# Performance work log

Measured on AMD Instinct MI355X. Metric: run time of the kernel, lower is better.

## Reference

```python
import jax, jax.numpy as jnp
import numpy as np

B, D, H, E, L = 8192, 1024, 1024, 16, 2  # batch, input_dim, exp_hidden_dim, exp_num, exp_layers


def setup_inputs() -> dict:
    key = jax.random.key(0)
    ks = jax.random.split(key, 12)
    s_in = 1.0 / np.sqrt(D)
    s_h = 1.0 / np.sqrt(H)
    return {
        "x":   jax.random.normal(ks[0], (B, D), dtype=jnp.float32),
        # per-expert embedding layer (E experts fused on leading axis)
        "W1":  jax.random.uniform(ks[1], (E, D, H), jnp.float32, -s_in, s_in),
        "b1":  jax.random.uniform(ks[2], (E, H), jnp.float32, -s_in, s_in),
        # per-expert hidden layer (shared across the L repeated blocks, as in the torch code)
        "W2":  jax.random.uniform(ks[3], (E, H, H), jnp.float32, -s_h, s_h),
        "b2":  jax.random.uniform(ks[4], (E, H), jnp.float32, -s_h, s_h),
        # per-expert output layer H -> 1
        "Wo":  jax.random.uniform(ks[5], (E, H), jnp.float32, -s_h, s_h),
        "bo":  jax.random.uniform(ks[6], (E,), jnp.float32, -s_h, s_h),
        # two gates: D -> E, softmax
        "Wg1": jax.random.uniform(ks[7], (D, E), jnp.float32, -s_in, s_in),
        "bg1": jax.random.uniform(ks[8], (E,), jnp.float32, -s_in, s_in),
        "Wg2": jax.random.uniform(ks[9], (D, E), jnp.float32, -s_in, s_in),
        "bg2": jax.random.uniform(ks[10], (E,), jnp.float32, -s_in, s_in),
    }


def reference(x, W1, b1, W2, b2, Wo, bo, Wg1, bg1, Wg2, bg2):
    # Batched experts: h [B, E, H]
    h = jax.nn.sigmoid(jnp.einsum("bd,edh->beh", x, W1) + b1)
    for _ in range(L):  # weight-shared hidden blocks (ReLU then the SAME linear)
        h = jnp.einsum("beh,ehk->bek", jax.nn.relu(h), W2) + b2
    f = jnp.einsum("beh,eh->be", h, Wo) + bo  # expert scalar outputs [B, E]
    g1 = jax.nn.softmax(x @ Wg1 + bg1, axis=-1)  # [B, E]
    g2 = jax.nn.softmax(x @ Wg2 + bg2, axis=-1)
    out1 = jnp.einsum("be,be->b", g1, f)
    out2 = jnp.einsum("be,be->b", g2, f)
    return (out1, out2)
```

## Files before the change

### kernel.cpp

```cpp
#include <hip/hip_runtime.h>
#include <hip/hip_bf16.h>
#include <cstdint>
#include <cstddef>


using half8   = __attribute__((ext_vector_type(8))) _Float16;
using floatx4 = __attribute__((ext_vector_type(4))) float;

template<int ACT>
__global__ __launch_bounds__(256, 3)
void gemm_kernel(const _Float16* __restrict__ A, const _Float16* __restrict__ Bt,
                 const float* __restrict__ bias, _Float16* __restrict__ C,
                 size_t a_estride,
                 const float* __restrict__ Wo, float* __restrict__ f, int e0)
{
    __shared__ __align__(16) _Float16 sbuf[2][16 * 512];

    const int tid  = threadIdx.x;
    const int lane = tid & 63;
    const int w    = tid >> 6;
    const int wm   = w & 1;
    const int wn   = w >> 1;

    const int g    = gridDim.z;
    const int flat = blockIdx.x + (blockIdx.y << 3) + (blockIdx.z << 9);
    const int xcd  = flat & 7;
    int s = flat >> 3;
    int le, mb_base;
    if (g <= 8) {
        const int p = 8 / g;
        le = xcd / p;
        mb_base = (xcd % p) * (64 / p);
    } else {
        le = (xcd << 1) | (s >> 9);
        s &= 511;
        mb_base = 0;
    }
    const int nb = (s >> 2) & 7;
    const int mb = mb_base + (s >> 5) * 4 + (s & 3);
    const int m0 = mb * 128;
    const int n0 = nb * 128;

    const _Float16* Ae = A   + (size_t)le * a_estride;
    const _Float16* Be = Bt  + (size_t)le * (1024ull * 1024ull);
    const float*    be = bias + (size_t)le * 1024ull;
    _Float16*       Ce = C   + (size_t)le * (8192ull * 1024ull);

    const int mtb_blk = m0 >> 4;
    const int ntb_blk = n0 >> 4;
    const int mtb = mtb_blk + wm * 4;

    const _Float16* gs[4];
#pragma unroll
    for (int u = 0; u < 4; ++u) {
        const int fidx = w * 4 + u;
        gs[u] = (fidx < 8)
            ? (Ae + (size_t)(mtb_blk + fidx) * (32 * 512) + lane * 8)
            : (Be + (size_t)(ntb_blk + (fidx - 8)) * (32 * 512) + lane * 8);
    }

    floatx4 acc[4][4];
#pragma unroll
    for (int i = 0; i < 4; ++i)
#pragma unroll
        for (int j = 0; j < 4; ++j) { floatx4 z = {0.f, 0.f, 0.f, 0.f}; acc[i][j] = z; }

    auto STAGE = [&](_Float16* buf) {
#pragma unroll
        for (int u = 0; u < 4; ++u) {
            __builtin_amdgcn_global_load_lds(
                (const __attribute__((address_space(1))) void*)gs[u],
                (__attribute__((address_space(3))) void*)(buf + (w * 4 + u) * 512),
                16, 0, 0);
            gs[u] += 512;
        }
    };
    auto COMPUTE = [&](const _Float16* buf) {
        half8 a[4], b[4];
#pragma unroll
        for (int i = 0; i < 4; ++i)
            a[i] = *(const half8*)(buf + (wm * 4 + i) * 512 + lane * 8);
#pragma unroll
        for (int j = 0; j < 4; ++j)
            b[j] = *(const half8*)(buf + 4096 + (wn * 4 + j) * 512 + lane * 8);
#pragma unroll
        for (int i = 0; i < 4; ++i)
#pragma unroll
            for (int j = 0; j < 4; ++j)
                acc[i][j] = __builtin_amdgcn_mfma_f32_16x16x32_f16(a[i], b[j], acc[i][j], 0, 0, 0);
    };

    STAGE(sbuf[0]);
    __syncthreads();
#pragma unroll 1
    for (int c = 0; c < 30; c += 2) {
        STAGE(sbuf[1]);
        COMPUTE(sbuf[0]);
        __syncthreads();
        STAGE(sbuf[0]);
        COMPUTE(sbuf[1]);
        __syncthreads();
    }
    STAGE(sbuf[1]);
    COMPUTE(sbuf[0]);
    __syncthreads();
    COMPUTE(sbuf[1]);

    const int q   = lane >> 4;
    const int l15 = lane & 15;
    float bj[4];
#pragma unroll
    for (int j = 0; j < 4; ++j) bj[j] = be[n0 + wn * 64 + j * 16 + l15];

    if (ACT == 2) {
        const float* we = Wo + (size_t)(e0 + le) * 1024;
        float wj[4];
#pragma unroll
        for (int j = 0; j < 4; ++j) wj[j] = we[n0 + wn * 64 + j * 16 + l15];
#pragma unroll
        for (int i = 0; i < 4; ++i) {
            const int mbase = m0 + wm * 64 + i * 16 + q * 4;
#pragma unroll
            for (int r = 0; r < 4; ++r) {
                float sacc = 0.f;
#pragma unroll
                for (int j = 0; j < 4; ++j)
                    sacc += fmaxf(acc[i][j][r] + bj[j], 0.0f) * wj[j];
#pragma unroll
                for (int m = 1; m < 16; m <<= 1) sacc += __shfl_xor(sacc, m, 64);
                if (l15 == 0) atomicAdd(&f[(size_t)(mbase + r) * 16 + (e0 + le)], sacc);
            }
        }
    } else {
        __syncthreads();
        _Float16* T = &sbuf[0][0] + w * (32 * 72);
        const int kcg0 = ((n0 + wn * 64) >> 5);
#pragma unroll
        for (int p = 0; p < 2; ++p) {
#pragma unroll
            for (int i2 = 0; i2 < 2; ++i2) {
                const int i = p * 2 + i2;
#pragma unroll
                for (int r = 0; r < 4; ++r) {
                    const int row = i2 * 16 + q * 4 + r;
#pragma unroll
                    for (int j = 0; j < 4; ++j) {
                        float v = acc[i][j][r] + bj[j];
                        v = 1.0f / (1.0f + __expf(-v));
                        T[row * 72 + j * 16 + l15] = (_Float16)v;
                    }
                }
            }
#pragma unroll
            for (int i2 = 0; i2 < 2; ++i2) {
                const int i = p * 2 + i2;
                const int mt = mtb + i;
#pragma unroll
                for (int kci = 0; kci < 2; ++kci) {
                    half8 v = *(const half8*)(T + (i2 * 16 + l15) * 72 + kci * 32 + q * 8);
                    *(half8*)(Ce + ((size_t)mt * 32 + kcg0 + kci) * 512 + lane * 8) = v;
                }
            }
        }
    }
}

__global__ __launch_bounds__(256)
void castx_kernel(const float* __restrict__ x, _Float16* __restrict__ xb)
{
    __shared__ _Float16 tile[64 * 72];
    const int k0 = blockIdx.x * 64;
    const int m0 = blockIdx.y * 64;
    const int tid = threadIdx.x;
    const int col4 = (tid & 15) * 4;
    const int rb   = tid >> 4;
#pragma unroll
    for (int p = 0; p < 4; ++p) {
        const int row = rb + p * 16;
        float4 a = *(const float4*)(x + (size_t)(m0 + row) * 1024 + k0 + col4);
        _Float16* d = tile + row * 72 + col4;
        d[0] = (_Float16)a.x; d[1] = (_Float16)a.y; d[2] = (_Float16)a.z; d[3] = (_Float16)a.w;
    }
    __syncthreads();
    const int lane = tid & 63, w = tid >> 6;
    const int l15 = lane & 15, q = lane >> 4;
#pragma unroll
    for (int ff = 0; ff < 2; ++ff) {
        const int fidx = w * 2 + ff;
        const int mi = fidx >> 1, kci = fidx & 1;
        half8 v = *(const half8*)(tile + (mi * 16 + l15) * 72 + kci * 32 + q * 8);
        const size_t mt = (m0 >> 4) + mi, kc = (k0 >> 5) + kci;
        *(half8*)(xb + (mt * 32 + kc) * 512 + lane * 8) = v;
    }
}

__global__ __launch_bounds__(256)
void wtr_kernel(const float* __restrict__ W1, const float* __restrict__ W2,
                _Float16* __restrict__ W1F, _Float16* __restrict__ W2F,
                const float* __restrict__ Wo, float* __restrict__ v)
{
    __shared__ _Float16 tile[64 * 73];
    const int z = blockIdx.z;
    const float* src = (z < 16) ? (W1 + (size_t)z * 1048576ull) : (W2 + (size_t)(z - 16) * 1048576ull);
    _Float16*    dst = (z < 16) ? (W1F + (size_t)z * 1048576ull) : (W2F + (size_t)(z - 16) * 1048576ull);
    const int n0 = blockIdx.x * 64;
    const int k0 = blockIdx.y * 64;
    const int tid = threadIdx.x;
    const int lane = tid & 63, w = tid >> 6;
    const int l15 = lane & 15, q = lane >> 4;

    const int col4 = l15 * 4;
    const int rbase = w * 4 + q;
    float4 a4[4];
#pragma unroll
    for (int p = 0; p < 4; ++p) {
        const int row = rbase + p * 16;
        a4[p] = *(const float4*)(src + (size_t)(k0 + row) * 1024 + n0 + col4);
        _Float16* d = tile + row * 73 + col4;
        d[0] = (_Float16)a4[p].x; d[1] = (_Float16)a4[p].y;
        d[2] = (_Float16)a4[p].z; d[3] = (_Float16)a4[p].w;
    }

    if (z >= 16) {
        const int e = z - 16;
        const float* wo = Wo + ((size_t)e << 10) + n0;
        float* ve = v + ((size_t)e << 10) + k0;
#pragma unroll
        for (int p = 0; p < 4; ++p) {
            float s = a4[p].x * wo[col4] + a4[p].y * wo[col4 + 1]
                    + a4[p].z * wo[col4 + 2] + a4[p].w * wo[col4 + 3];
            s += __shfl_xor(s, 1, 64);
            s += __shfl_xor(s, 2, 64);
            s += __shfl_xor(s, 4, 64);
            s += __shfl_xor(s, 8, 64);
            if (l15 == 0) atomicAdd(&ve[rbase + p * 16], s);
        }
    }

    __syncthreads();
#pragma unroll
    for (int ff = 0; ff < 2; ++ff) {
        const int fidx = w * 2 + ff;
        const int nti = fidx >> 1, kci = fidx & 1;
        half8 hv;
#pragma unroll
        for (int jj = 0; jj < 8; ++jj)
            hv[jj] = tile[(kci * 32 + q * 8 + jj) * 73 + nti * 16 + l15];
        const size_t nt = (n0 >> 4) + nti, kc = (k0 >> 5) + kci;
        *(half8*)(dst + (nt * 32 + kc) * 512 + lane * 8) = hv;
    }
}

__global__ __launch_bounds__(256)
void zerof_kernel(float* __restrict__ f)
{
    const size_t i = ((size_t)blockIdx.x * 256 + threadIdx.x) * 4;
    float4 z = {0.f, 0.f, 0.f, 0.f};
    *(float4*)(f + i) = z;
}

__global__ __launch_bounds__(64)
void prep_bo2_kernel(const float* __restrict__ b2, const float* __restrict__ Wo,
                     const float* __restrict__ bo, float* __restrict__ bo2)
{
    const int e = blockIdx.x;
    const int lane = threadIdx.x;
    const float* br = b2 + ((size_t)e << 10);
    const float* wo = Wo + ((size_t)e << 10);
    float s = 0.f;
#pragma unroll
    for (int t = 0; t < 16; ++t) s += br[t * 64 + lane] * wo[t * 64 + lane];
#pragma unroll
    for (int m = 1; m < 64; m <<= 1) s += __shfl_xor(s, m, 64);
    if (lane == 0) bo2[e] = s + bo[e];
}

__global__ __launch_bounds__(256)
void final_kernel(const float* __restrict__ x,
                  const float* __restrict__ Wg1, const float* __restrict__ bg1,
                  const float* __restrict__ Wg2, const float* __restrict__ bg2,
                  const float* __restrict__ f, const float* __restrict__ bo2,
                  float* __restrict__ out)
{
    const int lane = threadIdx.x & 63;
    const int w    = threadIdx.x >> 6;
    const int b    = blockIdx.x * 8 + w * 2;
    const float* xA = x + (size_t)b * 1024;
    const float* xB = xA + 1024;
    float g1A[16], g2A[16], g1B[16], g2B[16];
#pragma unroll
    for (int e = 0; e < 16; ++e) { g1A[e] = 0.f; g2A[e] = 0.f; g1B[e] = 0.f; g2B[e] = 0.f; }
#pragma unroll 2
    for (int t = 0; t < 16; ++t) {
        const int d = t * 64 + lane;
        const float xa = xA[d];
        const float xb2 = xB[d];
        const float4* w1 = (const float4*)(Wg1 + (size_t)d * 16);
        const float4* w2 = (const float4*)(Wg2 + (size_t)d * 16);
#pragma unroll
        for (int q4 = 0; q4 < 4; ++q4) {
            const float4 c1 = w1[q4];
            const float4 c2 = w2[q4];
#pragma unroll
            for (int c = 0; c < 4; ++c) {
                const int e = q4 * 4 + c;
                const float v1 = (c == 0) ? c1.x : (c == 1) ? c1.y : (c == 2) ? c1.z : c1.w;
                const float v2 = (c == 0) ? c2.x : (c == 1) ? c2.y : (c == 2) ? c2.z : c2.w;
                g1A[e] += xa * v1; g1B[e] += xb2 * v1;
                g2A[e] += xa * v2; g2B[e] += xb2 * v2;
            }
        }
    }
#pragma unroll
    for (int e = 0; e < 16; ++e) {
#pragma unroll
        for (int m = 1; m < 64; m <<= 1) {
            g1A[e] += __shfl_xor(g1A[e], m, 64);
            g2A[e] += __shfl_xor(g2A[e], m, 64);
            g1B[e] += __shfl_xor(g1B[e], m, 64);
            g2B[e] += __shfl_xor(g2B[e], m, 64);
        }
    }
    const float* fbA = f + (size_t)b * 16;
    const float* fbB = fbA + 16;
#pragma unroll
    for (int rr = 0; rr < 2; ++rr) {
        const float* gp1 = rr ? g1B : g1A;
        const float* gp2 = rr ? g2B : g2A;
        const float* fb  = rr ? fbB : fbA;
        float a1[16], a2[16], m1 = -1e30f, m2 = -1e30f;
#pragma unroll
        for (int e = 0; e < 16; ++e) {
            a1[e] = gp1[e] + bg1[e]; m1 = fmaxf(m1, a1[e]);
            a2[e] = gp2[e] + bg2[e]; m2 = fmaxf(m2, a2[e]);
        }
        float s1 = 0.f, s2 = 0.f, o1 = 0.f, o2 = 0.f;
#pragma unroll
        for (int e = 0; e < 16; ++e) {
            a1[e] = __expf(a1[e] - m1); s1 += a1[e];
            a2[e] = __expf(a2[e] - m2); s2 += a2[e];
        }
#pragma unroll
        for (int e = 0; e < 16; ++e) {
            const float fe = fb[e] + bo2[e];
            o1 += a1[e] * fe; o2 += a2[e] * fe;
        }
        if (lane == 0) { out[b + rr] = o1 / s1; out[8192 + b + rr] = o2 / s2; }
    }
}

extern "C" void kernel_launch(void* const* d_in, const int* in_sizes, int n_in,
                              void* d_out, int out_size, void* d_ws, size_t ws_size,
                              hipStream_t stream)
{
    const float* x   = (const float*)d_in[0];
    const float* W1  = (const float*)d_in[1];
    const float* b1  = (const float*)d_in[2];
    const float* W2  = (const float*)d_in[3];
    const float* b2  = (const float*)d_in[4];
    const float* Wo  = (const float*)d_in[5];
    const float* bo  = (const float*)d_in[6];
    const float* Wg1 = (const float*)d_in[7];
    const float* bg1 = (const float*)d_in[8];
    const float* Wg2 = (const float*)d_in[9];
    const float* bg2 = (const float*)d_in[10];
    float* out = (float*)d_out;

    char* ws = (char*)d_ws;
    _Float16* xb  = (_Float16*)(ws);
    _Float16* W1F = (_Float16*)(ws + 16777216ull);
    _Float16* W2F = (_Float16*)(ws + 50331648ull);
    float*    f   = (float*)   (ws + 83886080ull);
    float*    v   = (float*)   (ws + 84410368ull);
    float*    bo2 = (float*)   (ws + 84475904ull);
    char* hbase = ws + 84475968ull;

    int g = 1;
    const int cands[4] = {16, 8, 4, 2};
    for (int ci = 0; ci < 4; ++ci) {
        const size_t need = 84475968ull + (size_t)cands[ci] * 16777216ull;
        if (need <= ws_size) { g = cands[ci]; break; }
    }
    _Float16* h0 = (_Float16*)hbase;

    zerof_kernel<<<144, 256, 0, stream>>>(f);
    castx_kernel<<<dim3(16, 128), 256, 0, stream>>>(x, xb);
    wtr_kernel<<<dim3(16, 16, 32), 256, 0, stream>>>(W1, W2, W1F, W2F, Wo, v);
    prep_bo2_kernel<<<16, 64, 0, stream>>>(b2, Wo, bo, bo2);

    for (int e0 = 0; e0 < 16; e0 += g) {
        gemm_kernel<0><<<dim3(8, 64, g), 256, 0, stream>>>(
            xb, W1F + (size_t)e0 * 1048576ull, b1 + (size_t)e0 * 1024, h0, 0,
            nullptr, nullptr, 0);
        gemm_kernel<2><<<dim3(8, 64, g), 256, 0, stream>>>(
            h0, W2F + (size_t)e0 * 1048576ull, b2 + (size_t)e0 * 1024, h0, 8192ull * 1024ull,
            v, f, e0);
    }
    final_kernel<<<1024, 256, 0, stream>>>(x, Wg1, bg1, Wg2, bg2, f, bo2, out);
}
```

Before: 838.5 us.

## Widen GEMM block tile to 128x256 for more B reuse per block

Each GEMM workgroup now computes a 128x256 output tile instead of 128x128. Each wave holds 4x8 MFMA accumulators, and the LDS staging buffer grows to 24 fragments per stage. The aim is higher arithmetic intensity, with fewer global/LDS loads per MFMA and half as many workgroups. In exchange, register pressure rises (launch bounds drop from 3 to 2 blocks per CU), the epilogue transpose is rewritten, and the grid indexing is flattened to 2D.

Result: faster. 784.3 us (-6.5%).

```diff
diff --git a/kernel.cpp b/kernel.cpp
--- a/kernel.cpp
+++ b/kernel.cpp
@@ -8,13 +8,13 @@
 using floatx4 = __attribute__((ext_vector_type(4))) float;
 
 template<int ACT>
-__global__ __launch_bounds__(256, 3)
+__global__ __launch_bounds__(256, 2)
 void gemm_kernel(const _Float16* __restrict__ A, const _Float16* __restrict__ Bt,
                  const float* __restrict__ bias, _Float16* __restrict__ C,
                  size_t a_estride,
                  const float* __restrict__ Wo, float* __restrict__ f, int e0)
 {
-    __shared__ __align__(16) _Float16 sbuf[2][16 * 512];
+    __shared__ __align__(16) _Float16 sbuf[2][24 * 512];
 
     const int tid  = threadIdx.x;
     const int lane = tid & 63;
@@ -22,71 +22,70 @@
     const int wm   = w & 1;
     const int wn   = w >> 1;
 
-    const int g    = gridDim.z;
-    const int flat = blockIdx.x + (blockIdx.y << 3) + (blockIdx.z << 9);
+    const int flat = blockIdx.x + (blockIdx.y << 3);
     const int xcd  = flat & 7;
     int s = flat >> 3;
+    const int g = gridDim.y >> 5;
     int le, mb_base;
     if (g <= 8) {
         const int p = 8 / g;
         le = xcd / p;
         mb_base = (xcd % p) * (64 / p);
     } else {
-        le = (xcd << 1) | (s >> 9);
-        s &= 511;
+        le = (xcd << 1) | (s >> 8);
+        s &= 255;
         mb_base = 0;
     }
-    const int nb = (s >> 2) & 7;
-    const int mb = mb_base + (s >> 5) * 4 + (s & 3);
+    const int nb = (s >> 2) & 3;
+    const int mb = mb_base + (s >> 4) * 4 + (s & 3);
     const int m0 = mb * 128;
-    const int n0 = nb * 128;
-
-    const _Float16* Ae = A   + (size_t)le * a_estride;
-    const _Float16* Be = Bt  + (size_t)le * (1024ull * 1024ull);
+    const int n0 = nb * 256;
+
+    const _Float16* Ae = A    + (size_t)le * a_estride;
+    const _Float16* Be = Bt   + (size_t)le * (1024ull * 1024ull);
     const float*    be = bias + (size_t)le * 1024ull;
-    _Float16*       Ce = C   + (size_t)le * (8192ull * 1024ull);
+    _Float16*       Ce = C    + (size_t)le * (8192ull * 1024ull);
 
     const int mtb_blk = m0 >> 4;
     const int ntb_blk = n0 >> 4;
-    const int mtb = mtb_blk + wm * 4;
-
-    const _Float16* gs[4];
-#pragma unroll
-    for (int u = 0; u < 4; ++u) {
-        const int fidx = w * 4 + u;
+
+    const _Float16* gs[6];
+#pragma unroll
+    for (int u = 0; u < 6; ++u) {
+        const int fidx = w * 6 + u;
         gs[u] = (fidx < 8)
             ? (Ae + (size_t)(mtb_blk + fidx) * (32 * 512) + lane * 8)
             : (Be + (size_t)(ntb_blk + (fidx - 8)) * (32 * 512) + lane * 8);
     }
 
-    floatx4 acc[4][4];
+    floatx4 acc[4][8];
 #pragma unroll
     for (int i = 0; i < 4; ++i)
 #pragma unroll
-        for (int j = 0; j < 4; ++j) { floatx4 z = {0.f, 0.f, 0.f, 0.f}; acc[i][j] = z; }
+        for (int j = 0; j < 8; ++j) { floatx4 z = {0.f, 0.f, 0.f, 0.f}; acc[i][j] = z; }
 
     auto STAGE = [&](_Float16* buf) {
 #pragma unroll
-        for (int u = 0; u < 4; ++u) {
+        for (int u = 0; u < 6; ++u) {
             __builtin_amdgcn_global_load_lds(
                 (const __attribute__((address_space(1))) void*)gs[u],
-                (__attribute__((address_space(3))) void*)(buf + (w * 4 + u) * 512),
+                (__attribute__((address_space(3))) void*)(buf + (w * 6 + u) * 512),
                 16, 0, 0);
             gs[u] += 512;
         }
     };
     auto COMPUTE = [&](const _Float16* buf) {
-        half8 a[4], b[4];
+        half8 a[4], b[8];
 #pragma unroll
         for (int i = 0; i < 4; ++i)
             a[i] = *(const half8*)(buf + (wm * 4 + i) * 512 + lane * 8);
 #pragma unroll
-        for (int j = 0; j < 4; ++j)
-            b[j] = *(const half8*)(buf + 4096 + (wn * 4 + j) * 512 + lane * 8);
+        for (int j = 0; j < 8; ++j)
+            b[j] = *(const half8*)(buf + 4096 + (wn * 8 + j) * 512 + lane * 8);
 #pragma unroll
         for (int i = 0; i < 4; ++i)
 #pragma unroll
-            for (int j = 0; j < 4; ++j)
+            for (int j = 0; j < 8; ++j)
                 acc[i][j] = __builtin_amdgcn_mfma_f32_16x16x32_f16(a[i], b[j], acc[i][j], 0, 0, 0);
     };
 
@@ -108,15 +107,15 @@
 
     const int q   = lane >> 4;
     const int l15 = lane & 15;
-    float bj[4];
-#pragma unroll
-    for (int j = 0; j < 4; ++j) bj[j] = be[n0 + wn * 64 + j * 16 + l15];
+    float bj[8];
+#pragma unroll
+    for (int j = 0; j < 8; ++j) bj[j] = be[n0 + wn * 128 + j * 16 + l15];
 
     if (ACT == 2) {
         const float* we = Wo + (size_t)(e0 + le) * 1024;
-        float wj[4];
-#pragma unroll
-        for (int j = 0; j < 4; ++j) wj[j] = we[n0 + wn * 64 + j * 16 + l15];
+        float wj[8];
+#pragma unroll
+        for (int j = 0; j < 8; ++j) wj[j] = we[n0 + wn * 128 + j * 16 + l15];
 #pragma unroll
         for (int i = 0; i < 4; ++i) {
             const int mbase = m0 + wm * 64 + i * 16 + q * 4;
@@ -124,7 +123,7 @@
             for (int r = 0; r < 4; ++r) {
                 float sacc = 0.f;
 #pragma unroll
-                for (int j = 0; j < 4; ++j)
+                for (int j = 0; j < 8; ++j)
                     sacc += fmaxf(acc[i][j][r] + bj[j], 0.0f) * wj[j];
 #pragma unroll
                 for (int m = 1; m < 16; m <<= 1) sacc += __shfl_xor(sacc, m, 64);
@@ -133,33 +132,23 @@
         }
     } else {
         __syncthreads();
-        _Float16* T = &sbuf[0][0] + w * (32 * 72);
-        const int kcg0 = ((n0 + wn * 64) >> 5);
-#pragma unroll
-        for (int p = 0; p < 2; ++p) {
-#pragma unroll
-            for (int i2 = 0; i2 < 2; ++i2) {
-                const int i = p * 2 + i2;
+        _Float16* T = &sbuf[0][0] + w * 3072;
+        const int kcg0 = (n0 + wn * 128) >> 5;
+#pragma unroll
+        for (int i = 0; i < 4; ++i) {
+#pragma unroll
+            for (int j = 0; j < 8; ++j)
 #pragma unroll
                 for (int r = 0; r < 4; ++r) {
-                    const int row = i2 * 16 + q * 4 + r;
-#pragma unroll
-                    for (int j = 0; j < 4; ++j) {
-                        float v = acc[i][j][r] + bj[j];
-                        v = 1.0f / (1.0f + __expf(-v));
-                        T[row * 72 + j * 16 + l15] = (_Float16)v;
-                    }
+                    float v = acc[i][j][r] + bj[j];
+                    v = 1.0f / (1.0f + __expf(-v));
+                    T[(q * 4 + r) * 136 + j * 16 + l15] = (_Float16)v;
                 }
-            }
-#pragma unroll
-            for (int i2 = 0; i2 < 2; ++i2) {
-                const int i = p * 2 + i2;
-                const int mt = mtb + i;
-#pragma unroll
-                for (int kci = 0; kci < 2; ++kci) {
-                    half8 v = *(const half8*)(T + (i2 * 16 + l15) * 72 + kci * 32 + q * 8);
-                    *(half8*)(Ce + ((size_t)mt * 32 + kcg0 + kci) * 512 + lane * 8) = v;
-                }
+            const int mt = mtb_blk + wm * 4 + i;
+#pragma unroll
+            for (int kci = 0; kci < 4; ++kci) {
+                half8 v8 = *(const half8*)(T + l15 * 136 + kci * 32 + q * 8);
+                *(half8*)(Ce + ((size_t)mt * 32 + kcg0 + kci) * 512 + lane * 8) = v8;
             }
         }
     }
@@ -389,10 +378,10 @@
     prep_bo2_kernel<<<16, 64, 0, stream>>>(b2, Wo, bo, bo2);
 
     for (int e0 = 0; e0 < 16; e0 += g) {
-        gemm_kernel<0><<<dim3(8, 64, g), 256, 0, stream>>>(
+        gemm_kernel<0><<<dim3(8, 32 * g), 256, 0, stream>>>(
             xb, W1F + (size_t)e0 * 1048576ull, b1 + (size_t)e0 * 1024, h0, 0,
             nullptr, nullptr, 0);
-        gemm_kernel<2><<<dim3(8, 64, g), 256, 0, stream>>>(
+        gemm_kernel<2><<<dim3(8, 32 * g), 256, 0, stream>>>(
             h0, W2F + (size_t)e0 * 1048576ull, b2 + (size_t)e0 * 1024, h0, 8192ull * 1024ull,
             v, f, e0);
     }
```
